# Optimization experiments

Hardware: AMD Instinct MI355X
Metric: run time of the kernel (lower is better)

## Reference

```python
import jax, jax.numpy as jnp
import numpy as np

B, C_IN, H, W, PAIR_DIM = 4, 23, 256, 512, 64


def setup_inputs() -> dict:
    key = jax.random.key(0)
    k1, k2, k3 = jax.random.split(key, 3)
    msa = jax.random.normal(k1, (B, C_IN, H, W), dtype=jnp.float32)
    # 1x1 Conv2d weight (out, in) and bias, Kaiming-ish scale
    W_conv = jax.random.normal(k2, (PAIR_DIM, C_IN), dtype=jnp.float32) * (1.0 / np.sqrt(C_IN))
    b_conv = jax.random.normal(k3, (PAIR_DIM,), dtype=jnp.float32) * 0.01
    return {"msa": msa, "W_conv": W_conv, "b_conv": b_conv}


def reference(msa, W_conv, b_conv):
    # 1x1 conv == per-position channel mixing: (B,23,H,W) -> (B,C,H,W)
    emb = jnp.einsum("oi,bihw->bohw", W_conv, msa) + b_conv[None, :, None, None]
    emb = jax.nn.relu(emb)
    # mean over MSA depth H distributes over the outer addition:
    # mean_H(emb[...,i,None] + emb[...,None,j]) == avg[...,i,None] + avg[...,None,j]
    avg = emb.mean(axis=2)  # (B, C, W)
    pairs = avg[:, :, :, None] + avg[:, :, None, :]  # (B, C, W, W)
    return jnp.transpose(pairs, (0, 2, 3, 1))  # (B, W, W, C)
```

## Files before the change

kernel.cpp:

```cpp
#include <hip/hip_runtime.h>

#define B_   4
#define CIN  23
#define H_   256
#define W_   512
#define CO   64
#define HC   8
#define NPART (B_ * W_ * CO)

typedef float f32x4 __attribute__((ext_vector_type(4)));
typedef _Float16 half8 __attribute__((ext_vector_type(8)));

__global__ __launch_bounds__(256) void conv_mfma_kernel(
    const float* __restrict__ msa,
    const float* __restrict__ Wc,
    const float* __restrict__ bias,
    float* __restrict__ partial)
{
    const int tid  = threadIdx.x;
    const int lane = tid & 63;
    const int mg   = tid >> 6;
    const int wrow = lane & 15;
    const int kg   = lane >> 4;

    const int wq = blockIdx.x;
    const int hc = blockIdx.y;
    const int b  = blockIdx.z;
    const int w0 = wq * 16;

    half8 afrag;
#pragma unroll
    for (int j = 0; j < 8; ++j) {
        const int k = 8 * kg + j;
        afrag[j] = (_Float16)((k < CIN) ? Wc[(16 * mg + wrow) * CIN + k] : 0.f);
    }
    float bias_r[4];
#pragma unroll
    for (int r = 0; r < 4; ++r) bias_r[r] = bias[16 * mg + 4 * kg + r];

    float acc0 = 0.f, acc1 = 0.f, acc2 = 0.f, acc3 = 0.f;

    __shared__ __align__(16) _Float16 xs[2][4][16][40];
    for (int t = tid; t < 2 * 4 * 16 * 40; t += 256)
        (&xs[0][0][0][0])[t] = (_Float16)0.f;

    const size_t HW = (size_t)H_ * W_;

    auto STAGE = [&](int s, int bufi) {
        const int hg = hc * 32 + s * 4 + mg;
        const float* src = msa + ((size_t)b * CIN) * HW + (size_t)hg * W_ + w0 + wrow;
#pragma unroll
        for (int m = 0; m < 6; ++m) {
            const int i = kg + 4 * m;
            if (i < CIN)
                xs[bufi][mg][wrow][i] = (_Float16)src[(size_t)i * HW];
        }
    };

    STAGE(0, 0);
    __syncthreads();

#pragma unroll 2
    for (int s = 0; s < 8; ++s) {
        const int cur = s & 1;
        if (s < 7) STAGE(s + 1, cur ^ 1);
#pragma unroll
        for (int hh = 0; hh < 4; ++hh) {
            const half8 bfrag = *(const half8*)&xs[cur][hh][wrow][8 * kg];
            f32x4 c = {0.f, 0.f, 0.f, 0.f};
            c = __builtin_amdgcn_mfma_f32_16x16x32_f16(afrag, bfrag, c, 0, 0, 0);
            acc0 += fmaxf(c[0] + bias_r[0], 0.f);
            acc1 += fmaxf(c[1] + bias_r[1], 0.f);
            acc2 += fmaxf(c[2] + bias_r[2], 0.f);
            acc3 += fmaxf(c[3] + bias_r[3], 0.f);
        }
        __syncthreads();
    }

    f32x4 v; v[0] = acc0; v[1] = acc1; v[2] = acc2; v[3] = acc3;
    float* dst = partial + (((size_t)hc * B_ + b) * W_ + w0 + wrow) * CO + 16 * mg + 4 * kg;
    *(f32x4*)dst = v;
}

__global__ __launch_bounds__(256) void reduce_avg_kernel(
    const float* __restrict__ partial,
    float* __restrict__ avg)
{
    const int idx = blockIdx.x * 256 + threadIdx.x;
    const f32x4* p4 = (const f32x4*)partial;
    f32x4 s = p4[idx];
#pragma unroll
    for (int k = 1; k < HC; ++k) s += p4[(size_t)k * (NPART / 4) + idx];
    ((f32x4*)avg)[idx] = s * (1.0f / H_);
}

__global__ __launch_bounds__(256) void pairs_kernel(
    const float* __restrict__ avg,
    float* __restrict__ out)
{
    const int b   = blockIdx.y;
    const int wi  = blockIdx.x;
    const int tid = threadIdx.x;
    const int cq  = tid & 15;
    const int wj0 = tid >> 4;

    const f32x4* a4 = (const f32x4*)avg;
    const f32x4 aI = a4[(b * W_ + wi) * 16 + cq];
    f32x4* o4 = (f32x4*)out + ((size_t)(b * W_ + wi)) * W_ * 16;

#pragma unroll 4
    for (int wj = wj0; wj < W_; wj += 16) {
        const f32x4 aJ = a4[(b * W_ + wj) * 16 + cq];
        o4[(size_t)wj * 16 + cq] = aI + aJ;
    }
}

extern "C" void kernel_launch(void* const* d_in, const int* in_sizes, int n_in,
                              void* d_out, int out_size, void* d_ws, size_t ws_size,
                              hipStream_t stream) {
    const float* msa = (const float*)d_in[0];
    const float* Wc  = (const float*)d_in[1];
    const float* bc  = (const float*)d_in[2];
    float* out = (float*)d_out;
    float* avg = (float*)d_ws;

    float* partial = (float*)d_out;

    conv_mfma_kernel<<<dim3(32, HC, B_), 256, 0, stream>>>(msa, Wc, bc, partial);
    reduce_avg_kernel<<<dim3(NPART / 4 / 256), 256, 0, stream>>>(partial, avg);
    pairs_kernel<<<dim3(W_, B_), 256, 0, stream>>>(avg, out);
}
```

Measured before the change: 69.26 us.

## Widen conv tile to 32 columns and split H into 16 chunks

```diff
diff --git a/kernel.cpp b/kernel.cpp
--- a/kernel.cpp
+++ b/kernel.cpp
@@ -5,7 +5,7 @@
 #define H_   256
 #define W_   512
 #define CO   64
-#define HC   8
+#define HC   16
 #define NPART (B_ * W_ * CO)
 
 typedef float f32x4 __attribute__((ext_vector_type(4)));
@@ -22,11 +22,13 @@
     const int mg   = tid >> 6;
     const int wrow = lane & 15;
     const int kg   = lane >> 4;
+    const int wl   = lane & 31;
+    const int cp   = lane >> 5;
 
     const int wq = blockIdx.x;
     const int hc = blockIdx.y;
     const int b  = blockIdx.z;
-    const int w0 = wq * 16;
+    const int w0 = wq * 32;
 
     half8 afrag;
 #pragma unroll
@@ -38,48 +40,59 @@
 #pragma unroll
     for (int r = 0; r < 4; ++r) bias_r[r] = bias[16 * mg + 4 * kg + r];
 
-    float acc0 = 0.f, acc1 = 0.f, acc2 = 0.f, acc3 = 0.f;
+    float acc[2][4];
+#pragma unroll
+    for (int q = 0; q < 2; ++q)
+#pragma unroll
+        for (int r = 0; r < 4; ++r) acc[q][r] = 0.f;
 
-    __shared__ __align__(16) _Float16 xs[2][4][16][40];
-    for (int t = tid; t < 2 * 4 * 16 * 40; t += 256)
+    __shared__ __align__(16) _Float16 xs[2][4][32][40];
+    for (int t = tid; t < 2 * 4 * 32 * 40; t += 256)
         (&xs[0][0][0][0])[t] = (_Float16)0.f;
+    __syncthreads();
 
     const size_t HW = (size_t)H_ * W_;
 
     auto STAGE = [&](int s, int bufi) {
-        const int hg = hc * 32 + s * 4 + mg;
-        const float* src = msa + ((size_t)b * CIN) * HW + (size_t)hg * W_ + w0 + wrow;
+        const int hg = hc * 16 + s * 4 + mg;
+        const float* src = msa + ((size_t)b * CIN) * HW + (size_t)hg * W_ + w0 + wl;
 #pragma unroll
-        for (int m = 0; m < 6; ++m) {
-            const int i = kg + 4 * m;
+        for (int m = 0; m < 12; ++m) {
+            const int i = cp + 2 * m;
             if (i < CIN)
-                xs[bufi][mg][wrow][i] = (_Float16)src[(size_t)i * HW];
+                xs[bufi][mg][wl][i] = (_Float16)src[(size_t)i * HW];
         }
     };
 
     STAGE(0, 0);
     __syncthreads();
 
-#pragma unroll 2
-    for (int s = 0; s < 8; ++s) {
+#pragma unroll
+    for (int s = 0; s < 4; ++s) {
         const int cur = s & 1;
-        if (s < 7) STAGE(s + 1, cur ^ 1);
+        if (s < 3) STAGE(s + 1, cur ^ 1);
 #pragma unroll
         for (int hh = 0; hh < 4; ++hh) {
-            const half8 bfrag = *(const half8*)&xs[cur][hh][wrow][8 * kg];
-            f32x4 c = {0.f, 0.f, 0.f, 0.f};
-            c = __builtin_amdgcn_mfma_f32_16x16x32_f16(afrag, bfrag, c, 0, 0, 0);
-            acc0 += fmaxf(c[0] + bias_r[0], 0.f);
-            acc1 += fmaxf(c[1] + bias_r[1], 0.f);
-            acc2 += fmaxf(c[2] + bias_r[2], 0.f);
-            acc3 += fmaxf(c[3] + bias_r[3], 0.f);
+#pragma unroll
+            for (int q = 0; q < 2; ++q) {
+                const half8 bfrag = *(const half8*)&xs[cur][hh][q * 16 + wrow][8 * kg];
+                f32x4 c = {0.f, 0.f, 0.f, 0.f};
+                c = __builtin_amdgcn_mfma_f32_16x16x32_f16(afrag, bfrag, c, 0, 0, 0);
+#pragma unroll
+                for (int r = 0; r < 4; ++r)
+                    acc[q][r] += fmaxf(c[r] + bias_r[r], 0.f);
+            }
         }
         __syncthreads();
     }
 
-    f32x4 v; v[0] = acc0; v[1] = acc1; v[2] = acc2; v[3] = acc3;
-    float* dst = partial + (((size_t)hc * B_ + b) * W_ + w0 + wrow) * CO + 16 * mg + 4 * kg;
-    *(f32x4*)dst = v;
+#pragma unroll
+    for (int q = 0; q < 2; ++q) {
+        f32x4 v; v[0] = acc[q][0]; v[1] = acc[q][1]; v[2] = acc[q][2]; v[3] = acc[q][3];
+        float* dst = partial + (((size_t)hc * B_ + b) * W_ + w0 + q * 16 + wrow) * CO
+                   + 16 * mg + 4 * kg;
+        *(f32x4*)dst = v;
+    }
 }
 
 __global__ __launch_bounds__(256) void reduce_avg_kernel(
@@ -126,7 +139,7 @@
 
     float* partial = (float*)d_out;
 
-    conv_mfma_kernel<<<dim3(32, HC, B_), 256, 0, stream>>>(msa, Wc, bc, partial);
+    conv_mfma_kernel<<<dim3(16, HC, B_), 256, 0, stream>>>(msa, Wc, bc, partial);
     reduce_avg_kernel<<<dim3(NPART / 4 / 256), 256, 0, stream>>>(partial, avg);
     pairs_kernel<<<dim3(W_, B_), 256, 0, stream>>>(avg, out);
 }
```

New measurement: 79.62 us. 15.0% more time.
